# Kernel optimization log

Measured on AMD Instinct MI355X. Metric: run time of the kernel, lower is better.

## Reference

```python
import jax, jax.numpy as jnp
import numpy as np

B, L, D, H = 4, 2048, 1024, 8
DH = D // H
NEG = float(-2**32 + 1)  # padding value used by the torch module


def setup_inputs() -> dict:
    key = jax.random.key(0)
    ks = jax.random.split(key, 7)
    queries = jax.random.normal(ks[0], (B, L, D), dtype=jnp.float32)
    keys = jax.random.normal(ks[1], (B, L, D), dtype=jnp.float32)
    sequence_length = jax.random.randint(ks[2], (B,), 1, L + 1, dtype=jnp.int32)
    scale = 0.02
    W_q = jax.random.normal(ks[3], (D, D), dtype=jnp.float32) * scale
    W_k = jax.random.normal(ks[4], (D, D), dtype=jnp.float32) * scale
    W_v = jax.random.normal(ks[5], (D, D), dtype=jnp.float32) * scale
    W_o = jax.random.normal(ks[6], (D, D), dtype=jnp.float32) * scale
    return {"queries": queries, "keys": keys, "sequence_length": sequence_length,
            "W_q": W_q, "W_k": W_k, "W_v": W_v, "W_o": W_o}


def reference(queries, keys, sequence_length, W_q, W_k, W_v, W_o):
    b, lq, d = queries.shape
    lk = keys.shape[1]
    # projections (nn.Linear, no bias): x @ W.T
    Q = (queries @ W_q.T).reshape(b, lq, H, DH).transpose(2, 0, 1, 3)  # (H,B,Lq,dh)
    K = (keys @ W_k.T).reshape(b, lk, H, DH).transpose(2, 0, 1, 3)
    V = (keys @ W_v.T).reshape(b, lk, H, DH).transpose(2, 0, 1, 3)
    scores = jnp.einsum('hbqd,hbkd->hbqk', Q, K) / jnp.sqrt(jnp.float32(DH))
    # additive key mask: positions >= sequence_length get large negative
    key_mask = jnp.arange(lk)[None, :] < sequence_length[:, None]      # (B,Lk)
    scores = jnp.where(key_mask[None, :, None, :], scores, NEG)
    attn = jax.nn.softmax(scores, axis=-1)
    # post-softmax multiplicative query mask
    q_mask = (jnp.arange(lq)[None, :] < sequence_length[:, None]).astype(attn.dtype)  # (B,Lq)
    attn = attn * q_mask[None, :, :, None]
    out = jnp.einsum('hbqk,hbkd->hbqd', attn, V)                       # (H,B,Lq,dh)
    # chunk-cat order: head h occupies columns h*dh:(h+1)*dh
    out = out.transpose(1, 2, 0, 3).reshape(b, lq, d)
    return out @ W_o.T  # dropout_rate=0 -> identity
```

## Files before the change

### kernel.cpp

```cpp
#include <hip/hip_runtime.h>
#include <math.h>

constexpr int Bsz = 4;
constexpr int Lsz = 2048;
constexpr int Dsz = 1024;
constexpr int Hn  = 8;
constexpr int Dh  = 128;
constexpr int GM  = Bsz * Lsz;
constexpr int GK  = Dsz;

typedef __attribute__((ext_vector_type(8))) short bf16x8;
typedef __attribute__((ext_vector_type(4))) float f32x4;

union FragU { unsigned int u[4]; bf16x8 f; };

__device__ __forceinline__ void gload16(const void* g, void* l) {
    __builtin_amdgcn_global_load_lds(
        (const __attribute__((address_space(1))) unsigned int*)g,
        (__attribute__((address_space(3))) unsigned int*)l, 16, 0, 0);
}

__device__ __forceinline__ void split2(float f0, float f1,
                                       unsigned int& hp, unsigned int& lp) {
    unsigned int u0 = __float_as_uint(f0), u1 = __float_as_uint(f1);
    hp = (u0 >> 16) | (u1 & 0xffff0000u);
    float l0 = f0 - __uint_as_float(u0 & 0xffff0000u);
    float l1 = f1 - __uint_as_float(u1 & 0xffff0000u);
    lp = (__float_as_uint(l0) >> 16) | (__float_as_uint(l1) & 0xffff0000u);
}

__device__ __forceinline__ void split4(float4 f, ushort4& h, ushort4& l2) {
    unsigned int ux = __float_as_uint(f.x), uy = __float_as_uint(f.y),
                 uz = __float_as_uint(f.z), uw = __float_as_uint(f.w);
    h.x = (unsigned short)(ux >> 16); h.y = (unsigned short)(uy >> 16);
    h.z = (unsigned short)(uz >> 16); h.w = (unsigned short)(uw >> 16);
    float lx = f.x - __uint_as_float(ux & 0xffff0000u);
    float ly = f.y - __uint_as_float(uy & 0xffff0000u);
    float lz = f.z - __uint_as_float(uz & 0xffff0000u);
    float lw = f.w - __uint_as_float(uw & 0xffff0000u);
    l2.x = (unsigned short)(__float_as_uint(lx) >> 16);
    l2.y = (unsigned short)(__float_as_uint(ly) >> 16);
    l2.z = (unsigned short)(__float_as_uint(lz) >> 16);
    l2.w = (unsigned short)(__float_as_uint(lw) >> 16);
}

struct WConv4 {
    const float4* w[4];
    ushort4* h[4];
    ushort4* l[4];
    float s[4];
};

__global__ __launch_bounds__(256) void conv_w4(WConv4 a) {
    int wi = blockIdx.x >> 10;
    int i = (blockIdx.x & 1023) * 256 + threadIdx.x;
    float4 f = a.w[wi][i];
    float s = a.s[wi];
    f.x *= s; f.y *= s; f.z *= s; f.w *= s;
    ushort4 h, l;
    split4(f, h, l);
    a.h[wi][i] = h; a.l[wi][i] = l;
}

__global__ __launch_bounds__(256) void gemm_qkv(
    const float* __restrict__ Aq, const float* __restrict__ Ak,
    const ushort* __restrict__ Wfh, const ushort* __restrict__ Wfl,
    ushort* __restrict__ Qhi, ushort* __restrict__ Qlo,
    ushort* __restrict__ Khi, ushort* __restrict__ Klo,
    ushort* __restrict__ Vthi, ushort* __restrict__ Vtlo,
    const int* __restrict__ slen)
{
    const int tid = threadIdx.x;
    const int bm = blockIdx.y << 7;
    const int bn = blockIdx.x << 7;
    const int grp = bn >> 10;

    const int nk = slen[bm >> 11];
    if ((bm & (Lsz - 1)) >= nk) return;

    __shared__ float  As[128 * 32];
    __shared__ ushort Bh_s[128 * 32];
    __shared__ ushort Bl_s[128 * 32];

    const float* A = (grp == 0) ? Aq : Ak;

    const int w  = tid >> 6;
    const int l  = tid & 63;
    const int wm = w & 1;
    const int wn = w >> 1;

    const float* agp[4]; float* alp[4];
#pragma unroll
    for (int i = 0; i < 4; ++i) {
        int s = i * 256 + tid;
        int row = ((s >> 7) << 4) + (s & 15);
        int kk  = (((s >> 4) & 3) << 3) + (((s >> 6) & 1) << 2);
        agp[i] = A + (size_t)(bm + row) * GK + kk;
        alp[i] = &As[s * 4];
    }
    const ushort* bgh[2]; const ushort* bgl[2]; ushort* blh[2]; ushort* bll[2];
#pragma unroll
    for (int i = 0; i < 2; ++i) {
        int s = i * 256 + tid;
        int row = ((s >> 6) << 4) + (s & 15);
        int kk  = ((s >> 4) & 3) << 3;
        bgh[i] = Wfh + (size_t)(bn + row) * GK + kk;
        bgl[i] = Wfl + (size_t)(bn + row) * GK + kk;
        blh[i] = &Bh_s[s * 8];
        bll[i] = &Bl_s[s * 8];
    }

    f32x4 acc[4][4];
#pragma unroll
    for (int i = 0; i < 4; ++i)
#pragma unroll
        for (int j = 0; j < 4; ++j) acc[i][j] = (f32x4)0.f;

    for (int k0 = 0; k0 < GK; k0 += 32) {
#pragma unroll
        for (int i = 0; i < 4; ++i) gload16(agp[i] + k0, alp[i]);
#pragma unroll
        for (int i = 0; i < 2; ++i) {
            gload16(bgh[i] + k0, blh[i]);
            gload16(bgl[i] + k0, bll[i]);
        }
        __syncthreads();

        FragU ah[4], al4[4];
        bf16x8 bhf[4], blf[4];
#pragma unroll
        for (int fn = 0; fn < 4; ++fn) {
            int fng = wn * 4 + fn;
            bhf[fn] = *(const bf16x8*)&Bh_s[(fng * 64 + l) * 8];
            blf[fn] = *(const bf16x8*)&Bl_s[(fng * 64 + l) * 8];
        }
#pragma unroll
        for (int fm = 0; fm < 4; ++fm) {
            int fmg = wm * 4 + fm;
            float4 fa0 = *(const float4*)&As[(fmg * 128 + l) * 4];
            float4 fa1 = *(const float4*)&As[(fmg * 128 + 64 + l) * 4];
            split2(fa0.x, fa0.y, ah[fm].u[0], al4[fm].u[0]);
            split2(fa0.z, fa0.w, ah[fm].u[1], al4[fm].u[1]);
            split2(fa1.x, fa1.y, ah[fm].u[2], al4[fm].u[2]);
            split2(fa1.z, fa1.w, ah[fm].u[3], al4[fm].u[3]);
        }

#pragma unroll
        for (int fm = 0; fm < 4; ++fm)
#pragma unroll
            for (int fn = 0; fn < 4; ++fn) {
                acc[fm][fn] = __builtin_amdgcn_mfma_f32_16x16x32_bf16(
                    ah[fm].f, bhf[fn], acc[fm][fn], 0, 0, 0);
                acc[fm][fn] = __builtin_amdgcn_mfma_f32_16x16x32_bf16(
                    ah[fm].f, blf[fn], acc[fm][fn], 0, 0, 0);
                acc[fm][fn] = __builtin_amdgcn_mfma_f32_16x16x32_bf16(
                    al4[fm].f, bhf[fn], acc[fm][fn], 0, 0, 0);
            }
        __syncthreads();
    }

    const int rq = (l >> 4) << 2;
    const int cq = l & 15;
    ushort* OH = (grp == 0) ? Qhi : Khi;
    ushort* OL = (grp == 0) ? Qlo : Klo;
#pragma unroll
    for (int fm = 0; fm < 4; ++fm) {
        int r0 = bm + wm * 64 + fm * 16 + rq;
#pragma unroll
        for (int fn = 0; fn < 4; ++fn) {
            int cn = (bn & 1023) + wn * 64 + fn * 16 + cq;
            if (grp < 2) {
#pragma unroll
                for (int r = 0; r < 4; ++r) {
                    float f = acc[fm][fn][r];
                    unsigned int u = __float_as_uint(f);
                    float res = f - __uint_as_float(u & 0xffff0000u);
                    OH[(size_t)(r0 + r) * Dsz + cn] = (unsigned short)(u >> 16);
                    OL[(size_t)(r0 + r) * Dsz + cn] =
                        (unsigned short)(__float_as_uint(res) >> 16);
                }
            } else {
                ushort4 h4, l4;
                unsigned short* hp = (unsigned short*)&h4;
                unsigned short* lp = (unsigned short*)&l4;
#pragma unroll
                for (int r = 0; r < 4; ++r) {
                    float f = acc[fm][fn][r];
                    unsigned int u = __float_as_uint(f);
                    float res = f - __uint_as_float(u & 0xffff0000u);
                    hp[r] = (unsigned short)(u >> 16);
                    lp[r] = (unsigned short)(__float_as_uint(res) >> 16);
                }
                *(ushort4*)&Vthi[(size_t)cn * GM + r0] = h4;
                *(ushort4*)&Vtlo[(size_t)cn * GM + r0] = l4;
            }
        }
    }
}

__global__ __launch_bounds__(256) void gemm_o(
    const ushort* __restrict__ Ahi, const ushort* __restrict__ Alo,
    const ushort* __restrict__ Bhi, const ushort* __restrict__ Blo,
    float* __restrict__ C, const int* __restrict__ slen)
{
    const int tid = threadIdx.x;
    const int bm = blockIdx.y << 7;
    const int bn = blockIdx.x << 7;

    const int nk = slen[bm >> 11];
    if ((bm & (Lsz - 1)) >= nk) {
        int row = tid >> 1;
        int cb  = (tid & 1) << 6;
        float4 z = make_float4(0.f, 0.f, 0.f, 0.f);
        float4* cp = (float4*)(C + (size_t)(bm + row) * Dsz + bn + cb);
#pragma unroll
        for (int i = 0; i < 16; ++i) cp[i] = z;
        return;
    }

    __shared__ ushort Ah_s[128 * 32];
    __shared__ ushort Al_s[128 * 32];
    __shared__ ushort Bh_s[128 * 32];
    __shared__ ushort Bl_s[128 * 32];

    const int w  = tid >> 6;
    const int l  = tid & 63;
    const int wm = w & 1;
    const int wn = w >> 1;

    const ushort* agh[2]; const ushort* agl[2]; ushort* alh[2]; ushort* all2[2];
    const ushort* bgh[2]; const ushort* bgl[2]; ushort* blh[2]; ushort* bll[2];
#pragma unroll
    for (int i = 0; i < 2; ++i) {
        int s = i * 256 + tid;
        int row = ((s >> 6) << 4) + (s & 15);
        int kk  = ((s >> 4) & 3) << 3;
        agh[i] = Ahi + (size_t)(bm + row) * GK + kk;
        agl[i] = Alo + (size_t)(bm + row) * GK + kk;
        bgh[i] = Bhi + (size_t)(bn + row) * GK + kk;
        bgl[i] = Blo + (size_t)(bn + row) * GK + kk;
        alh[i] = &Ah_s[s * 8];  all2[i] = &Al_s[s * 8];
        blh[i] = &Bh_s[s * 8];  bll[i]  = &Bl_s[s * 8];
    }

    f32x4 acc[4][4];
#pragma unroll
    for (int i = 0; i < 4; ++i)
#pragma unroll
        for (int j = 0; j < 4; ++j) acc[i][j] = (f32x4)0.f;

    for (int k0 = 0; k0 < GK; k0 += 32) {
#pragma unroll
        for (int i = 0; i < 2; ++i) {
            gload16(agh[i] + k0, alh[i]);
            gload16(agl[i] + k0, all2[i]);
            gload16(bgh[i] + k0, blh[i]);
            gload16(bgl[i] + k0, bll[i]);
        }
        __syncthreads();

        bf16x8 ah[4], al4[4], bhf[4], blf[4];
#pragma unroll
        for (int f = 0; f < 4; ++f) {
            int fmg = wm * 4 + f;
            int fng = wn * 4 + f;
            ah[f]  = *(const bf16x8*)&Ah_s[(fmg * 64 + l) * 8];
            al4[f] = *(const bf16x8*)&Al_s[(fmg * 64 + l) * 8];
            bhf[f] = *(const bf16x8*)&Bh_s[(fng * 64 + l) * 8];
            blf[f] = *(const bf16x8*)&Bl_s[(fng * 64 + l) * 8];
        }

#pragma unroll
        for (int fm = 0; fm < 4; ++fm)
#pragma unroll
            for (int fn = 0; fn < 4; ++fn) {
                acc[fm][fn] = __builtin_amdgcn_mfma_f32_16x16x32_bf16(
                    ah[fm], bhf[fn], acc[fm][fn], 0, 0, 0);
                acc[fm][fn] = __builtin_amdgcn_mfma_f32_16x16x32_bf16(
                    ah[fm], blf[fn], acc[fm][fn], 0, 0, 0);
                acc[fm][fn] = __builtin_amdgcn_mfma_f32_16x16x32_bf16(
                    al4[fm], bhf[fn], acc[fm][fn], 0, 0, 0);
            }
        __syncthreads();
    }

    const int rq = (l >> 4) << 2;
    const int cq = l & 15;
#pragma unroll
    for (int fm = 0; fm < 4; ++fm) {
        int r0 = bm + wm * 64 + fm * 16 + rq;
#pragma unroll
        for (int fn = 0; fn < 4; ++fn) {
            int c0 = bn + wn * 64 + fn * 16 + cq;
#pragma unroll
            for (int r = 0; r < 4; ++r)
                C[(size_t)(r0 + r) * Dsz + c0] = acc[fm][fn][r];
        }
    }
}

__global__ __launch_bounds__(512) void flash_mfma(
    const ushort* __restrict__ Qhi, const ushort* __restrict__ Qlo,
    const ushort* __restrict__ Khi, const ushort* __restrict__ Klo,
    const ushort* __restrict__ Vthi, const ushort* __restrict__ Vtlo,
    const int* __restrict__ slen,
    ushort* __restrict__ Ohi, ushort* __restrict__ Olo)
{
    __shared__ __align__(16) ushort Ks[32 * 256];
    __shared__ __align__(16) ushort Vs[128 * 64];
    __shared__ __align__(16) unsigned int Pb[8 * 16 * 36];

    const int tid = threadIdx.x;
    const int w = tid >> 6, l = tid & 63;
    const int lg = l >> 4, lc = l & 15;
    const int q0 = blockIdx.x << 7;
    const int h = blockIdx.y, b = blockIdx.z;
    const int nk = slen[b];

    if (q0 >= nk) return;

    bf16x8 qh[4], ql[4];
    {
        size_t base = (size_t)(b * Lsz + q0 + (w << 4) + lc) * Dsz + h * Dh + lg * 8;
#pragma unroll
        for (int s = 0; s < 4; ++s) {
            qh[s] = *(const bf16x8*)&Qhi[base + s * 32];
            ql[s] = *(const bf16x8*)&Qlo[base + s * 32];
        }
    }

    const ushort* ksrc[2]; int klds[2];
    const ushort* vsrc[2]; int vlds[2];
#pragma unroll
    for (int i = 0; i < 2; ++i) {
        int s = i * 512 + tid;
        int j = s >> 5, p = s & 31;
        int lg4 = (p & 15) ^ (j & 15);
        const ushort* base = (p & 16) ? Klo : Khi;
        ksrc[i] = base + (size_t)(b * Lsz + j) * Dsz + h * Dh + lg4 * 8;
        klds[i] = s * 8;
    }
#pragma unroll
    for (int i = 0; i < 2; ++i) {
        int s = i * 512 + tid;
        int d = s >> 3, p = s & 7;
        int lgc = p ^ (d & 7);
        const ushort* base = (lgc & 4) ? Vtlo : Vthi;
        vsrc[i] = base + (size_t)(h * Dh + d) * (Bsz * Lsz) + b * Lsz + (lgc & 3) * 8;
        vlds[i] = s * 8;
    }

    f32x4 oacc[8];
#pragma unroll
    for (int fd = 0; fd < 8; ++fd) oacc[fd] = (f32x4)0.f;
    float lsum[4] = {0.f, 0.f, 0.f, 0.f};
    const int pbase = w * (16 * 36);

    for (int kb = 0; kb < nk; kb += 32) {
#pragma unroll
        for (int i = 0; i < 2; ++i) gload16(ksrc[i] + (size_t)kb * Dsz, &Ks[klds[i]]);
#pragma unroll
        for (int i = 0; i < 2; ++i) gload16(vsrc[i] + kb, &Vs[vlds[i]]);
        __syncthreads();

        f32x4 sa[2] = {(f32x4)0.f, (f32x4)0.f};
#pragma unroll
        for (int fn = 0; fn < 2; ++fn) {
            int j = fn * 16 + lc;
            int ro = j * 256;
#pragma unroll
            for (int s = 0; s < 4; ++s) {
                int phys = (s * 4 + lg) ^ (j & 15);
                bf16x8 kh = *(const bf16x8*)&Ks[ro + phys * 8];
                bf16x8 kl = *(const bf16x8*)&Ks[ro + 128 + phys * 8];
                sa[fn] = __builtin_amdgcn_mfma_f32_16x16x32_bf16(qh[s], kh, sa[fn], 0, 0, 0);
                sa[fn] = __builtin_amdgcn_mfma_f32_16x16x32_bf16(qh[s], kl, sa[fn], 0, 0, 0);
                sa[fn] = __builtin_amdgcn_mfma_f32_16x16x32_bf16(ql[s], kh, sa[fn], 0, 0, 0);
            }
        }

        if (kb + 32 > nk) {
#pragma unroll
            for (int fn = 0; fn < 2; ++fn) {
                bool oob = (kb + fn * 16 + lc) >= nk;
#pragma unroll
                for (int rr = 0; rr < 4; ++rr)
                    sa[fn][rr] = oob ? -1e30f : sa[fn][rr];
            }
        }

#pragma unroll
        for (int fn = 0; fn < 2; ++fn)
#pragma unroll
            for (int rr = 0; rr < 4; ++rr) {
                float p = __expf(sa[fn][rr]);
                lsum[rr] += p;
                unsigned int u = __float_as_uint(p);
                float res = p - __uint_as_float(u & 0xffff0000u);
                unsigned int lo16 = __float_as_uint(res) >> 16;
                Pb[pbase + (lg * 4 + rr) * 36 + fn * 16 + lc] =
                    (lo16 << 16) | (u >> 16);
            }

        const unsigned int* pr = &Pb[pbase + lc * 36 + lg * 8];
        uint4 a0 = *(const uint4*)pr;
        uint4 a1 = *(const uint4*)(pr + 4);
        FragU PH, PL;
        PH.u[0] = (a0.x & 0xffffu) | (a0.y << 16);
        PH.u[1] = (a0.z & 0xffffu) | (a0.w << 16);
        PH.u[2] = (a1.x & 0xffffu) | (a1.y << 16);
        PH.u[3] = (a1.z & 0xffffu) | (a1.w << 16);
        PL.u[0] = (a0.x >> 16) | (a0.y & 0xffff0000u);
        PL.u[1] = (a0.z >> 16) | (a0.w & 0xffff0000u);
        PL.u[2] = (a1.x >> 16) | (a1.y & 0xffff0000u);
        PL.u[3] = (a1.z >> 16) | (a1.w & 0xffff0000u);

#pragma unroll
        for (int fd = 0; fd < 8; ++fd) {
            int d = fd * 16 + lc;
            int ro = d * 64;
            int ph = lg ^ (d & 7);
            int pl2 = (4 + lg) ^ (d & 7);
            bf16x8 vh = *(const bf16x8*)&Vs[ro + ph * 8];
            bf16x8 vl = *(const bf16x8*)&Vs[ro + pl2 * 8];
            oacc[fd] = __builtin_amdgcn_mfma_f32_16x16x32_bf16(PH.f, vh, oacc[fd], 0, 0, 0);
            oacc[fd] = __builtin_amdgcn_mfma_f32_16x16x32_bf16(PH.f, vl, oacc[fd], 0, 0, 0);
            oacc[fd] = __builtin_amdgcn_mfma_f32_16x16x32_bf16(PL.f, vh, oacc[fd], 0, 0, 0);
        }
        __syncthreads();
    }

#pragma unroll
    for (int m = 1; m < 16; m <<= 1)
#pragma unroll
        for (int rr = 0; rr < 4; ++rr)
            lsum[rr] += __shfl_xor(lsum[rr], m, 64);

#pragma unroll
    for (int rr = 0; rr < 4; ++rr) {
        int q = q0 + (w << 4) + (lg << 2) + rr;
        bool valid = q < nk;
        float inv = valid ? (1.f / lsum[rr]) : 0.f;
        size_t base = (size_t)(b * Lsz + q) * Dsz + h * Dh + lc;
#pragma unroll
        for (int fd = 0; fd < 8; ++fd) {
            float val = valid ? oacc[fd][rr] * inv : 0.f;
            unsigned int u = __float_as_uint(val);
            float res = val - __uint_as_float(u & 0xffff0000u);
            Ohi[base + fd * 16] = (unsigned short)(u >> 16);
            Olo[base + fd * 16] = (unsigned short)(__float_as_uint(res) >> 16);
        }
    }
}

extern "C" void kernel_launch(void* const* d_in, const int* in_sizes, int n_in,
                              void* d_out, int out_size, void* d_ws, size_t ws_size,
                              hipStream_t stream) {
    (void)in_sizes; (void)n_in; (void)out_size; (void)ws_size;
    const float* queries = (const float*)d_in[0];
    const float* keys    = (const float*)d_in[1];
    const int*   slen    = (const int*)d_in[2];
    const float* Wq      = (const float*)d_in[3];
    const float* Wk      = (const float*)d_in[4];
    const float* Wv      = (const float*)d_in[5];
    const float* Wo      = (const float*)d_in[6];
    float* out = (float*)d_out;

    const size_t MD = (size_t)Bsz * Lsz * Dsz;
    const size_t WD = (size_t)Dsz * Dsz;
    ushort* Qhi  = (ushort*)d_ws;
    ushort* Qlo  = Qhi + MD;
    ushort* Khi  = Qlo + MD;
    ushort* Klo  = Khi + MD;
    ushort* Vthi = Klo + MD;
    ushort* Vtlo = Vthi + MD;
    ushort* Wfh  = Vtlo + MD;
    ushort* Wfl  = Wfh + 3 * WD;
    ushort* Woh  = Wfl + 3 * WD;
    ushort* Wol  = Woh + WD;

    const float scaleQ = 0.08838834764831845f;
    WConv4 wa;
    wa.w[0] = (const float4*)Wq; wa.h[0] = (ushort4*)Wfh;            wa.l[0] = (ushort4*)Wfl;            wa.s[0] = scaleQ;
    wa.w[1] = (const float4*)Wk; wa.h[1] = (ushort4*)(Wfh + WD);     wa.l[1] = (ushort4*)(Wfl + WD);     wa.s[1] = 1.f;
    wa.w[2] = (const float4*)Wv; wa.h[2] = (ushort4*)(Wfh + 2 * WD); wa.l[2] = (ushort4*)(Wfl + 2 * WD); wa.s[2] = 1.f;
    wa.w[3] = (const float4*)Wo; wa.h[3] = (ushort4*)Woh;            wa.l[3] = (ushort4*)Wol;            wa.s[3] = 1.f;
    conv_w4<<<4096, 256, 0, stream>>>(wa);

    gemm_qkv<<<dim3(24, 64), 256, 0, stream>>>(
        queries, keys, Wfh, Wfl, Qhi, Qlo, Khi, Klo, Vthi, Vtlo, slen);

    dim3 ga(Lsz / 128, Hn, Bsz);
    flash_mfma<<<ga, 512, 0, stream>>>(Qhi, Qlo, Khi, Klo, Vthi, Vtlo, slen,
                                       Qhi, Qlo );

    gemm_o<<<dim3(8, 64), 256, 0, stream>>>(Qhi, Qlo, Woh, Wol, out, slen);
}
```

Baseline: 431.0 us.

## Fuse weight bf16 split into GEMMs and widen QKV tile to 128x256

Removes the separate weight-conversion kernel, so the QKV and output GEMMs now load fp32 weights directly and split them into hi/lo bf16 fragments in registers, folding the Q scale into the activation split. The QKV GEMM moves to 512-thread blocks with a 256-wide N tile, halving the grid. This saves a launch and the writes and rereads of converted weights, but adds per-tile split ALU work (repeated across M tiles) and doubles the fp32 B-tile LDS traffic.

New measurement: 437.9 us. Within noise of the previous version (+1.6%).

```diff
diff --git a/kernel.cpp b/kernel.cpp
--- a/kernel.cpp
+++ b/kernel.cpp
@@ -29,42 +29,20 @@
     lp = (__float_as_uint(l0) >> 16) | (__float_as_uint(l1) & 0xffff0000u);
 }
 
-__device__ __forceinline__ void split4(float4 f, ushort4& h, ushort4& l2) {
-    unsigned int ux = __float_as_uint(f.x), uy = __float_as_uint(f.y),
-                 uz = __float_as_uint(f.z), uw = __float_as_uint(f.w);
-    h.x = (unsigned short)(ux >> 16); h.y = (unsigned short)(uy >> 16);
-    h.z = (unsigned short)(uz >> 16); h.w = (unsigned short)(uw >> 16);
-    float lx = f.x - __uint_as_float(ux & 0xffff0000u);
-    float ly = f.y - __uint_as_float(uy & 0xffff0000u);
-    float lz = f.z - __uint_as_float(uz & 0xffff0000u);
-    float lw = f.w - __uint_as_float(uw & 0xffff0000u);
-    l2.x = (unsigned short)(__float_as_uint(lx) >> 16);
-    l2.y = (unsigned short)(__float_as_uint(ly) >> 16);
-    l2.z = (unsigned short)(__float_as_uint(lz) >> 16);
-    l2.w = (unsigned short)(__float_as_uint(lw) >> 16);
-}
-
-struct WConv4 {
-    const float4* w[4];
-    ushort4* h[4];
-    ushort4* l[4];
-    float s[4];
-};
-
-__global__ __launch_bounds__(256) void conv_w4(WConv4 a) {
-    int wi = blockIdx.x >> 10;
-    int i = (blockIdx.x & 1023) * 256 + threadIdx.x;
-    float4 f = a.w[wi][i];
-    float s = a.s[wi];
-    f.x *= s; f.y *= s; f.z *= s; f.w *= s;
-    ushort4 h, l;
-    split4(f, h, l);
-    a.h[wi][i] = h; a.l[wi][i] = l;
-}
-
-__global__ __launch_bounds__(256) void gemm_qkv(
+__device__ __forceinline__ void frag_from_f32(float4 a, float4 b, float s,
+                                              FragU& H, FragU& L) {
+    a.x *= s; a.y *= s; a.z *= s; a.w *= s;
+    b.x *= s; b.y *= s; b.z *= s; b.w *= s;
+    split2(a.x, a.y, H.u[0], L.u[0]);
+    split2(a.z, a.w, H.u[1], L.u[1]);
+    split2(b.x, b.y, H.u[2], L.u[2]);
+    split2(b.z, b.w, H.u[3], L.u[3]);
+}
+
+__global__ __launch_bounds__(512, 4) void gemm_qkv(
     const float* __restrict__ Aq, const float* __restrict__ Ak,
-    const ushort* __restrict__ Wfh, const ushort* __restrict__ Wfl,
+    const float* __restrict__ Wq, const float* __restrict__ Wk,
+    const float* __restrict__ Wv,
     ushort* __restrict__ Qhi, ushort* __restrict__ Qlo,
     ushort* __restrict__ Khi, ushort* __restrict__ Klo,
     ushort* __restrict__ Vthi, ushort* __restrict__ Vtlo,
@@ -72,42 +50,41 @@
 {
     const int tid = threadIdx.x;
     const int bm = blockIdx.y << 7;
-    const int bn = blockIdx.x << 7;
+    const int bn = blockIdx.x << 8;
     const int grp = bn >> 10;
 
     const int nk = slen[bm >> 11];
     if ((bm & (Lsz - 1)) >= nk) return;
 
-    __shared__ float  As[128 * 32];
-    __shared__ ushort Bh_s[128 * 32];
-    __shared__ ushort Bl_s[128 * 32];
+    __shared__ float As[128 * 32];
+    __shared__ float Bs[256 * 32];
 
     const float* A = (grp == 0) ? Aq : Ak;
+    const float* W = (grp == 0) ? Wq : ((grp == 1) ? Wk : Wv);
+    const float ascale = (grp == 0) ? 0.08838834764831845f : 1.f;
 
     const int w  = tid >> 6;
     const int l  = tid & 63;
     const int wm = w & 1;
     const int wn = w >> 1;
 
-    const float* agp[4]; float* alp[4];
-#pragma unroll
-    for (int i = 0; i < 4; ++i) {
-        int s = i * 256 + tid;
+    const float* agp[2]; float* alp[2];
+#pragma unroll
+    for (int i = 0; i < 2; ++i) {
+        int s = i * 512 + tid;
         int row = ((s >> 7) << 4) + (s & 15);
         int kk  = (((s >> 4) & 3) << 3) + (((s >> 6) & 1) << 2);
         agp[i] = A + (size_t)(bm + row) * GK + kk;
         alp[i] = &As[s * 4];
     }
-    const ushort* bgh[2]; const ushort* bgl[2]; ushort* blh[2]; ushort* bll[2];
-#pragma unroll
-    for (int i = 0; i < 2; ++i) {
-        int s = i * 256 + tid;
-        int row = ((s >> 6) << 4) + (s & 15);
-        int kk  = ((s >> 4) & 3) << 3;
-        bgh[i] = Wfh + (size_t)(bn + row) * GK + kk;
-        bgl[i] = Wfl + (size_t)(bn + row) * GK + kk;
-        blh[i] = &Bh_s[s * 8];
-        bll[i] = &Bl_s[s * 8];
+    const float* bgp[4]; float* blp[4];
+#pragma unroll
+    for (int i = 0; i < 4; ++i) {
+        int s = i * 512 + tid;
+        int col = ((s >> 7) << 4) + (s & 15);
+        int kk  = (((s >> 4) & 3) << 3) + (((s >> 6) & 1) << 2);
+        bgp[i] = W + (size_t)((bn & 1023) + col) * GK + kk;
+        blp[i] = &Bs[s * 4];
     }
 
     f32x4 acc[4][4];
@@ -118,44 +95,36 @@
 
     for (int k0 = 0; k0 < GK; k0 += 32) {
 #pragma unroll
-        for (int i = 0; i < 4; ++i) gload16(agp[i] + k0, alp[i]);
-#pragma unroll
-        for (int i = 0; i < 2; ++i) {
-            gload16(bgh[i] + k0, blh[i]);
-            gload16(bgl[i] + k0, bll[i]);
-        }
-        __syncthreads();
-
-        FragU ah[4], al4[4];
-        bf16x8 bhf[4], blf[4];
+        for (int i = 0; i < 2; ++i) gload16(agp[i] + k0, alp[i]);
+#pragma unroll
+        for (int i = 0; i < 4; ++i) gload16(bgp[i] + k0, blp[i]);
+        __syncthreads();
+
+        FragU bh[4], bl[4];
 #pragma unroll
         for (int fn = 0; fn < 4; ++fn) {
             int fng = wn * 4 + fn;
-            bhf[fn] = *(const bf16x8*)&Bh_s[(fng * 64 + l) * 8];
-            blf[fn] = *(const bf16x8*)&Bl_s[(fng * 64 + l) * 8];
+            float4 b0 = *(const float4*)&Bs[(fng * 128 + l) * 4];
+            float4 b1 = *(const float4*)&Bs[(fng * 128 + 64 + l) * 4];
+            frag_from_f32(b0, b1, 1.f, bh[fn], bl[fn]);
         }
 #pragma unroll
         for (int fm = 0; fm < 4; ++fm) {
             int fmg = wm * 4 + fm;
-            float4 fa0 = *(const float4*)&As[(fmg * 128 + l) * 4];
-            float4 fa1 = *(const float4*)&As[(fmg * 128 + 64 + l) * 4];
-            split2(fa0.x, fa0.y, ah[fm].u[0], al4[fm].u[0]);
-            split2(fa0.z, fa0.w, ah[fm].u[1], al4[fm].u[1]);
-            split2(fa1.x, fa1.y, ah[fm].u[2], al4[fm].u[2]);
-            split2(fa1.z, fa1.w, ah[fm].u[3], al4[fm].u[3]);
-        }
-
-#pragma unroll
-        for (int fm = 0; fm < 4; ++fm)
+            float4 a0 = *(const float4*)&As[(fmg * 128 + l) * 4];
+            float4 a1 = *(const float4*)&As[(fmg * 128 + 64 + l) * 4];
+            FragU ah, al;
+            frag_from_f32(a0, a1, ascale, ah, al);
 #pragma unroll
             for (int fn = 0; fn < 4; ++fn) {
                 acc[fm][fn] = __builtin_amdgcn_mfma_f32_16x16x32_bf16(
-                    ah[fm].f, bhf[fn], acc[fm][fn], 0, 0, 0);
-                acc[fm][fn] = __builtin_amdgcn_mfma_f32_16x16x32_bf16(
-                    ah[fm].f, blf[fn], acc[fm][fn], 0, 0, 0);
-                acc[fm][fn] = __builtin_amdgcn_mfma_f32_16x16x32_bf16(
-                    al4[fm].f, bhf[fn], acc[fm][fn], 0, 0, 0);
-            }
+                    ah.f, bh[fn].f, acc[fm][fn], 0, 0, 0);
+                acc[fm][fn] = __builtin_amdgcn_mfma_f32_16x16x32_bf16(
+                    ah.f, bl[fn].f, acc[fm][fn], 0, 0, 0);
+                acc[fm][fn] = __builtin_amdgcn_mfma_f32_16x16x32_bf16(
+                    al.f, bh[fn].f, acc[fm][fn], 0, 0, 0);
+            }
+        }
         __syncthreads();
     }
 
@@ -200,7 +169,7 @@
 
 __global__ __launch_bounds__(256) void gemm_o(
     const ushort* __restrict__ Ahi, const ushort* __restrict__ Alo,
-    const ushort* __restrict__ Bhi, const ushort* __restrict__ Blo,
+    const float* __restrict__ Wo,
     float* __restrict__ C, const int* __restrict__ slen)
 {
     const int tid = threadIdx.x;
@@ -220,8 +189,7 @@
 
     __shared__ ushort Ah_s[128 * 32];
     __shared__ ushort Al_s[128 * 32];
-    __shared__ ushort Bh_s[128 * 32];
-    __shared__ ushort Bl_s[128 * 32];
+    __shared__ float  Bs[128 * 32];
 
     const int w  = tid >> 6;
     const int l  = tid & 63;
@@ -229,7 +197,6 @@
     const int wn = w >> 1;
 
     const ushort* agh[2]; const ushort* agl[2]; ushort* alh[2]; ushort* all2[2];
-    const ushort* bgh[2]; const ushort* bgl[2]; ushort* blh[2]; ushort* bll[2];
 #pragma unroll
     for (int i = 0; i < 2; ++i) {
         int s = i * 256 + tid;
@@ -237,10 +204,16 @@
         int kk  = ((s >> 4) & 3) << 3;
         agh[i] = Ahi + (size_t)(bm + row) * GK + kk;
         agl[i] = Alo + (size_t)(bm + row) * GK + kk;
-        bgh[i] = Bhi + (size_t)(bn + row) * GK + kk;
-        bgl[i] = Blo + (size_t)(bn + row) * GK + kk;
         alh[i] = &Ah_s[s * 8];  all2[i] = &Al_s[s * 8];
-        blh[i] = &Bh_s[s * 8];  bll[i]  = &Bl_s[s * 8];
+    }
+    const float* bgp[4]; float* blp[4];
+#pragma unroll
+    for (int i = 0; i < 4; ++i) {
+        int s = i * 256 + tid;
+        int col = ((s >> 7) << 4) + (s & 15);
+        int kk  = (((s >> 4) & 3) << 3) + (((s >> 6) & 1) << 2);
+        bgp[i] = Wo + (size_t)(bn + col) * GK + kk;
+        blp[i] = &Bs[s * 4];
     }
 
     f32x4 acc[4][4];
@@ -254,33 +227,35 @@
         for (int i = 0; i < 2; ++i) {
             gload16(agh[i] + k0, alh[i]);
             gload16(agl[i] + k0, all2[i]);
-            gload16(bgh[i] + k0, blh[i]);
-            gload16(bgl[i] + k0, bll[i]);
-        }
-        __syncthreads();
-
-        bf16x8 ah[4], al4[4], bhf[4], blf[4];
+        }
+#pragma unroll
+        for (int i = 0; i < 4; ++i) gload16(bgp[i] + k0, blp[i]);
+        __syncthreads();
+
+        bf16x8 ah[4], al4[4];
 #pragma unroll
         for (int f = 0; f < 4; ++f) {
             int fmg = wm * 4 + f;
-            int fng = wn * 4 + f;
             ah[f]  = *(const bf16x8*)&Ah_s[(fmg * 64 + l) * 8];
             al4[f] = *(const bf16x8*)&Al_s[(fmg * 64 + l) * 8];
-            bhf[f] = *(const bf16x8*)&Bh_s[(fng * 64 + l) * 8];
-            blf[f] = *(const bf16x8*)&Bl_s[(fng * 64 + l) * 8];
-        }
-
-#pragma unroll
-        for (int fm = 0; fm < 4; ++fm)
-#pragma unroll
-            for (int fn = 0; fn < 4; ++fn) {
-                acc[fm][fn] = __builtin_amdgcn_mfma_f32_16x16x32_bf16(
-                    ah[fm], bhf[fn], acc[fm][fn], 0, 0, 0);
-                acc[fm][fn] = __builtin_amdgcn_mfma_f32_16x16x32_bf16(
-                    ah[fm], blf[fn], acc[fm][fn], 0, 0, 0);
-                acc[fm][fn] = __builtin_amdgcn_mfma_f32_16x16x32_bf16(
-                    al4[fm], bhf[fn], acc[fm][fn], 0, 0, 0);
-            }
+        }
+#pragma unroll
+        for (int fn = 0; fn < 4; ++fn) {
+            int fng = wn * 4 + fn;
+            float4 b0 = *(const float4*)&Bs[(fng * 128 + l) * 4];
+            float4 b1 = *(const float4*)&Bs[(fng * 128 + 64 + l) * 4];
+            FragU bh, bl;
+            frag_from_f32(b0, b1, 1.f, bh, bl);
+#pragma unroll
+            for (int fm = 0; fm < 4; ++fm) {
+                acc[fm][fn] = __builtin_amdgcn_mfma_f32_16x16x32_bf16(
+                    ah[fm], bh.f, acc[fm][fn], 0, 0, 0);
+                acc[fm][fn] = __builtin_amdgcn_mfma_f32_16x16x32_bf16(
+                    ah[fm], bl.f, acc[fm][fn], 0, 0, 0);
+                acc[fm][fn] = __builtin_amdgcn_mfma_f32_16x16x32_bf16(
+                    al4[fm], bh.f, acc[fm][fn], 0, 0, 0);
+            }
+        }
         __syncthreads();
     }
 
@@ -467,32 +442,19 @@
     float* out = (float*)d_out;
 
     const size_t MD = (size_t)Bsz * Lsz * Dsz;
-    const size_t WD = (size_t)Dsz * Dsz;
     ushort* Qhi  = (ushort*)d_ws;
     ushort* Qlo  = Qhi + MD;
     ushort* Khi  = Qlo + MD;
     ushort* Klo  = Khi + MD;
     ushort* Vthi = Klo + MD;
     ushort* Vtlo = Vthi + MD;
-    ushort* Wfh  = Vtlo + MD;
-    ushort* Wfl  = Wfh + 3 * WD;
-    ushort* Woh  = Wfl + 3 * WD;
-    ushort* Wol  = Woh + WD;
-
-    const float scaleQ = 0.08838834764831845f;
-    WConv4 wa;
-    wa.w[0] = (const float4*)Wq; wa.h[0] = (ushort4*)Wfh;            wa.l[0] = (ushort4*)Wfl;            wa.s[0] = scaleQ;
-    wa.w[1] = (const float4*)Wk; wa.h[1] = (ushort4*)(Wfh + WD);     wa.l[1] = (ushort4*)(Wfl + WD);     wa.s[1] = 1.f;
-    wa.w[2] = (const float4*)Wv; wa.h[2] = (ushort4*)(Wfh + 2 * WD); wa.l[2] = (ushort4*)(Wfl + 2 * WD); wa.s[2] = 1.f;
-    wa.w[3] = (const float4*)Wo; wa.h[3] = (ushort4*)Woh;            wa.l[3] = (ushort4*)Wol;            wa.s[3] = 1.f;
-    conv_w4<<<4096, 256, 0, stream>>>(wa);
-
-    gemm_qkv<<<dim3(24, 64), 256, 0, stream>>>(
-        queries, keys, Wfh, Wfl, Qhi, Qlo, Khi, Klo, Vthi, Vtlo, slen);
+
+    gemm_qkv<<<dim3(12, 64), 512, 0, stream>>>(
+        queries, keys, Wq, Wk, Wv, Qhi, Qlo, Khi, Klo, Vthi, Vtlo, slen);
 
     dim3 ga(Lsz / 128, Hn, Bsz);
     flash_mfma<<<ga, 512, 0, stream>>>(Qhi, Qlo, Khi, Klo, Vthi, Vtlo, slen,
                                        Qhi, Qlo );
 
-    gemm_o<<<dim3(8, 64), 256, 0, stream>>>(Qhi, Qlo, Woh, Wol, out, slen);
-}
+    gemm_o<<<dim3(8, 64), 256, 0, stream>>>(Qhi, Qlo, Wo, out, slen);
+}
```
